# Performance work log

Hardware: AMD Instinct MI355X
Metric: run time of the kernel (lower is better)

## Reference

```python
import jax, jax.numpy as jnp
import numpy as np

H = 64        # hidden_dim
T = 3         # message passing steps
M = 3         # set2set steps
NEF = 4       # num_edge_features
NNF = 11      # num_node_features
NT = 12       # num_targets
N_NODES = 10000
N_EDGES = 50000
B = 256       # number of graphs


def setup_inputs() -> dict:
    key = jax.random.key(0)
    ks = jax.random.split(key, 32)

    def p(k, shape):
        fan_in = shape[-1]
        return jax.random.normal(k, shape, jnp.float32) / np.sqrt(fan_in)

    inp = {}
    inp['x'] = jax.random.normal(ks[0], (N_NODES, NNF), jnp.float32)
    inp['edge_attr'] = jax.random.uniform(ks[1], (N_EDGES, NEF), jnp.float32)
    inp['edge_index'] = jax.random.randint(ks[2], (2, N_EDGES), 0, N_NODES)
    inp['batch'] = jnp.sort(jax.random.randint(ks[3], (N_NODES,), 0, B))
    inp['batch_size'] = B
    # nn1: edge MLP -> per-edge HxH weight
    inp['w1a'] = p(ks[4], (H, NEF)); inp['b1a'] = jnp.zeros((H,), jnp.float32)
    inp['w1b'] = p(ks[5], (H, H));   inp['b1b'] = jnp.zeros((H,), jnp.float32)
    inp['w1c'] = p(ks[6], (H * H, H)); inp['b1c'] = jnp.zeros((H * H,), jnp.float32)
    # GRUCell
    inp['gru_wih'] = p(ks[7], (3 * H, H)); inp['gru_whh'] = p(ks[8], (3 * H, H))
    inp['gru_bih'] = jnp.zeros((3 * H,), jnp.float32); inp['gru_bhh'] = jnp.zeros((3 * H,), jnp.float32)
    # lin: (H + NNF) -> 2H
    inp['lin_w'] = p(ks[9], (2 * H, H + NNF)); inp['lin_b'] = jnp.zeros((2 * H,), jnp.float32)
    # Set2Set 2-layer LSTM: in_channels = 2H, input = 4H, hidden = 2H
    IC = 2 * H
    inp['lstm_wih0'] = p(ks[10], (4 * IC, 2 * IC)); inp['lstm_whh0'] = p(ks[11], (4 * IC, IC))
    inp['lstm_bih0'] = jnp.zeros((4 * IC,), jnp.float32); inp['lstm_bhh0'] = jnp.zeros((4 * IC,), jnp.float32)
    inp['lstm_wih1'] = p(ks[12], (4 * IC, IC)); inp['lstm_whh1'] = p(ks[13], (4 * IC, IC))
    inp['lstm_bih1'] = jnp.zeros((4 * IC,), jnp.float32); inp['lstm_bhh1'] = jnp.zeros((4 * IC,), jnp.float32)
    # nn2: 4H -> 8H -> num_targets
    inp['w2a'] = p(ks[14], (8 * H, 4 * H)); inp['b2a'] = jnp.zeros((8 * H,), jnp.float32)
    inp['w2b'] = p(ks[15], (NT, 8 * H)); inp['b2b'] = jnp.zeros((NT,), jnp.float32)
    return inp


def _gru(x, h, wih, whh, bih, bhh):
    gi = x @ wih.T + bih
    gh = h @ whh.T + bhh
    ir, iz, inn = jnp.split(gi, 3, axis=1)
    hr, hz, hn = jnp.split(gh, 3, axis=1)
    r = jax.nn.sigmoid(ir + hr)
    z = jax.nn.sigmoid(iz + hz)
    n = jnp.tanh(inn + r * hn)
    return (1.0 - z) * n + z * h


def _lstm(x, h, c, wih, whh, bih, bhh):
    g = x @ wih.T + bih + h @ whh.T + bhh
    i, f, gg, o = jnp.split(g, 4, axis=1)
    c_new = jax.nn.sigmoid(f) * c + jax.nn.sigmoid(i) * jnp.tanh(gg)
    h_new = jax.nn.sigmoid(o) * jnp.tanh(c_new)
    return h_new, c_new


def reference(x, edge_attr, w1a, b1a, w1b, b1b, w1c, b1c,
              gru_wih, gru_whh, gru_bih, gru_bhh, lin_w, lin_b,
              lstm_wih0, lstm_whh0, lstm_bih0, lstm_bhh0,
              lstm_wih1, lstm_whh1, lstm_bih1, lstm_bhh1,
              w2a, b2a, w2b, b2b, edge_index, batch, batch_size):
    N = x.shape[0]
    E = edge_attr.shape[0]
    src, dst = edge_index[0], edge_index[1]

    # pad node features into hidden state
    h = jnp.zeros((N, H), x.dtype).at[:, :x.shape[1]].set(x)

    # nn1 edge MLP -> per-edge (H, H) weight (edge_attr constant over T, hoisted)
    e1 = jax.nn.relu(edge_attr @ w1a.T + b1a)
    e1 = jax.nn.relu(e1 @ w1b.T + b1b)
    W_edge = (e1 @ w1c.T + b1c).reshape(E, H, H)  # [E, in, out]

    # T rounds of NNConv (gather -> per-edge matvec -> scatter-add) + GRU
    for _ in range(T):
        m_e = jnp.einsum('eh,eho->eo', h[src], W_edge)
        m = jax.ops.segment_sum(m_e, dst, num_segments=N)
        h = _gru(m, h, gru_wih, gru_whh, gru_bih, gru_bhh)

    h = jnp.concatenate([h, x], axis=1) @ lin_w.T + lin_b  # [N, 2H]

    # Set2Set readout with 2-layer LSTM
    IC = 2 * H
    q_star = jnp.zeros((batch_size, 2 * IC), h.dtype)
    h0 = jnp.zeros((batch_size, IC), h.dtype); c0 = jnp.zeros_like(h0)
    h1 = jnp.zeros_like(h0); c1 = jnp.zeros_like(h0)
    for _ in range(M):
        h0, c0 = _lstm(q_star, h0, c0, lstm_wih0, lstm_whh0, lstm_bih0, lstm_bhh0)
        h1, c1 = _lstm(h0, h1, c1, lstm_wih1, lstm_whh1, lstm_bih1, lstm_bhh1)
        q = h1  # [B, IC]
        e = jnp.sum(h * q[batch], axis=-1)  # [N]
        emax = jax.ops.segment_max(e, batch, num_segments=batch_size)
        a = jnp.exp(e - emax[batch])
        denom = jax.ops.segment_sum(a, batch, num_segments=batch_size)
        a = a / denom[batch]
        r = jax.ops.segment_sum(a[:, None] * h, batch, num_segments=batch_size)
        q_star = jnp.concatenate([q, r], axis=-1)  # [B, 4H]

    out = jax.nn.relu(q_star @ w2a.T + b2a) @ w2b.T + b2b
    return out
```

## Files before the change

kernel.cpp:

```cpp
#include <hip/hip_runtime.h>
#include <math.h>

#define NN 10000
#define NE 50000
#define BG 256
#define NNF 11
#define NT 12

typedef unsigned int u32;
typedef __attribute__((ext_vector_type(8))) short short8v;
typedef __attribute__((ext_vector_type(4))) float f32x4;

__device__ __forceinline__ float sigm(float x){ return 1.0f/(1.0f+__expf(-x)); }
__device__ __forceinline__ u32 f2bf(float f){
  u32 u = __float_as_uint(f);
  return (u + 0x7fffu + ((u>>16)&1u)) >> 16;
}
__device__ __forceinline__ float bf2f(u32 s){ return __uint_as_float(s<<16); }

__global__ __launch_bounds__(256) void k_h_init(const float* __restrict__ x, float* __restrict__ h,
                         unsigned short* __restrict__ hHi, unsigned short* __restrict__ hLo,
                         const float* __restrict__ b1c, float* __restrict__ hb,
                         float* __restrict__ m){
  __shared__ float sv[8][64];
  int t = threadIdx.x, w = t>>6, lane = t&63;
  int n0 = blockIdx.x*8 + w*2;
  #pragma unroll
  for (int q = 0; q < 2; ++q){
    int n = n0 + q;
    float v = (lane < NNF) ? x[n*NNF + lane] : 0.0f;
    h[n*64+lane] = v;
    u32 hv = f2bf(v);
    hHi[n*64+lane] = (unsigned short)hv;
    hLo[n*64+lane] = (unsigned short)f2bf(v - bf2f(hv));
    sv[2*w+q][lane] = v;
  }
  __syncthreads();
  #pragma unroll
  for (int q = 0; q < 2; ++q){
    int n = n0 + q;
    float acc = 0.f;
    #pragma unroll 8
    for (int i = 0; i < 64; ++i) acc = fmaf(sv[2*w+q][i], b1c[i*64+lane], acc);
    hb[n*64+lane] = acc;
    m[n*64+lane] = 0.f;
  }
}

__global__ void k_prep(const float* __restrict__ gwih, const float* __restrict__ gwhh,
                       const float* __restrict__ linw, const float* __restrict__ w1b,
                       const float* __restrict__ wih0, const float* __restrict__ whh0,
                       const float* __restrict__ wih1, const float* __restrict__ whh1,
                       const float* __restrict__ w2a,  const float* __restrict__ w1c,
                       float* __restrict__ wihT, float* __restrict__ whhT,
                       float* __restrict__ linT, unsigned short* __restrict__ w1bB,
                       float* __restrict__ p0i, float* __restrict__ p0h,
                       float* __restrict__ p1i, float* __restrict__ p1h,
                       float* __restrict__ w2aT, unsigned short* __restrict__ qtT,
                       int* __restrict__ deg, float* __restrict__ state0){
  int tid = blockIdx.x*256 + threadIdx.x;
  if (tid < 12288){ int i=tid>>6, j=tid&63; wihT[j*192+i]=gwih[tid]; return; }
  tid -= 12288;
  if (tid < 12288){ int i=tid>>6, j=tid&63; whhT[j*192+i]=gwhh[tid]; return; }
  tid -= 12288;
  if (tid < 9600){ int i=tid/75, j=tid-i*75; linT[j*128+i]=linw[tid]; return; }
  tid -= 9600;
  if (tid < 4096){ w1bB[tid] = (unsigned short)f2bf(w1b[tid]); return; }
  tid -= 4096;
  if (tid < 32768){ int i=tid>>7, j=tid&127;
    float4 v = make_float4(wih0[(j)*256+i], wih0[(128+j)*256+i],
                           wih0[(256+j)*256+i], wih0[(384+j)*256+i]);
    *(float4*)&p0i[tid*4] = v; return; }
  tid -= 32768;
  if (tid < 16384){ int i=tid>>7, j=tid&127;
    float4 v = make_float4(whh0[(j)*128+i], whh0[(128+j)*128+i],
                           whh0[(256+j)*128+i], whh0[(384+j)*128+i]);
    *(float4*)&p0h[tid*4] = v; return; }
  tid -= 16384;
  if (tid < 16384){ int i=tid>>7, j=tid&127;
    float4 v = make_float4(wih1[(j)*128+i], wih1[(128+j)*128+i],
                           wih1[(256+j)*128+i], wih1[(384+j)*128+i]);
    *(float4*)&p1i[tid*4] = v; return; }
  tid -= 16384;
  if (tid < 16384){ int i=tid>>7, j=tid&127;
    float4 v = make_float4(whh1[(j)*128+i], whh1[(128+j)*128+i],
                           whh1[(256+j)*128+i], whh1[(384+j)*128+i]);
    *(float4*)&p1h[tid*4] = v; return; }
  tid -= 16384;
  if (tid < 131072){ int i=tid>>8, j=tid&255; w2aT[j*512+i]=w2a[tid]; return; }
  tid -= 131072;
  if (tid < 262144){ int ko=tid>>6, hh=tid&63; int k=ko>>6, o=ko&63;
                     qtT[tid] = (unsigned short)f2bf(w1c[(hh*64+o)*64+k]); return; }
  tid -= 262144;
  if (tid < NN){ deg[tid] = 0; return; }
  tid -= NN;
  if (tid < 196608) state0[tid] = 0.f;
}

__global__ __launch_bounds__(256) void k_e1m(const float* __restrict__ ea,
                     const float* __restrict__ w1a, const float* __restrict__ b1a,
                     const unsigned short* __restrict__ w1bB, const float* __restrict__ b1b,
                     unsigned short* __restrict__ e1b){
  __shared__ unsigned short sHi[4][16][64], sLo[4][16][64];
  int t = threadIdx.x, w = t>>6, l = t&63;
  int c = l & 15, g = l >> 4;
  int eb = blockIdx.x*64 + w*16;
  float wa0=w1a[l*4+0], wa1=w1a[l*4+1], wa2=w1a[l*4+2], wa3=w1a[l*4+3];
  float bb1 = b1a[l];
  char* hbase = (char*)&sHi[w][0][0];
  char* lbase = (char*)&sLo[w][0][0];
  #pragma unroll
  for (int r = 0; r < 16; ++r){
    int e = eb + r; if (e >= NE) e = NE-1;
    float4 a = *(const float4*)&ea[e*4];
    float h1 = fmaxf(bb1 + a.x*wa0 + a.y*wa1 + a.z*wa2 + a.w*wa3, 0.f);
    u32 hv = f2bf(h1);
    u32 lv = f2bf(h1 - bf2f(hv));
    int wb = (r*128 + l*2) ^ ((r & 7) << 4);
    *(unsigned short*)(hbase + wb) = (unsigned short)hv;
    *(unsigned short*)(lbase + wb) = (unsigned short)lv;
  }
  __syncthreads();
  int xv = (c & 7) << 4;
  int rb0 = (c*128 + g*16) ^ xv;
  int rb1 = (c*128 + 64 + g*16) ^ xv;
  short8v aH0 = *(const short8v*)(hbase + rb0);
  short8v aH1 = *(const short8v*)(hbase + rb1);
  short8v aL0 = *(const short8v*)(lbase + rb0);
  short8v aL1 = *(const short8v*)(lbase + rb1);
  f32x4 acc[4];
  #pragma unroll
  for (int f = 0; f < 4; ++f){
    const short* wrow = (const short*)w1bB + (f*16 + c)*64 + g*8;
    short8v b0 = *(const short8v*)wrow;
    short8v b1 = *(const short8v*)(wrow + 32);
    acc[f] = f32x4{0.f,0.f,0.f,0.f};
    acc[f] = __builtin_amdgcn_mfma_f32_16x16x32_bf16(aH0, b0, acc[f], 0, 0, 0);
    acc[f] = __builtin_amdgcn_mfma_f32_16x16x32_bf16(aL0, b0, acc[f], 0, 0, 0);
    acc[f] = __builtin_amdgcn_mfma_f32_16x16x32_bf16(aH1, b1, acc[f], 0, 0, 0);
    acc[f] = __builtin_amdgcn_mfma_f32_16x16x32_bf16(aL1, b1, acc[f], 0, 0, 0);
  }
  #pragma unroll
  for (int f = 0; f < 4; ++f){
    float bb2 = b1b[f*16 + c];
    #pragma unroll
    for (int r = 0; r < 4; ++r){
      int e = eb + 4*g + r;
      if (e < NE)
        e1b[e*64 + f*16 + c] = (unsigned short)f2bf(fmaxf(acc[f][r] + bb2, 0.f));
    }
  }
}

__global__ __launch_bounds__(512) void k_P3(const unsigned short* __restrict__ hHi,
                      const unsigned short* __restrict__ hLo,
                      const unsigned short* __restrict__ qtT, u32* __restrict__ P2){
  __shared__ unsigned short sB[16384];
  int t = threadIdx.x; int w = t >> 6; int l = t & 63;
  int c = l & 15, g = l >> 4;
  int nt = blockIdx.x >> 4, kt = blockIdx.x & 15;
  int kob = kt*256;
  const char* qsrc = (const char*)qtT + (size_t)kob*128;
  char* sb = (char*)sB;
  #pragma unroll
  for (int r = 0; r < 4; ++r){
    int dstb = (r*512 + t)*16;
    int srcb = dstb ^ (((dstb >> 7) & 7) << 4);
    *(uint4*)(sb + dstb) = *(const uint4*)(qsrc + srcb);
  }
  int nb = nt*128 + w*16;
  int rowA = nb + c; if (rowA >= NN) rowA = NN-1;
  const short8v* aHiP = (const short8v*)((const short*)hHi + rowA*64 + g*8);
  const short8v* aLoP = (const short8v*)((const short*)hLo + rowA*64 + g*8);
  short8v aH0 = aHiP[0], aH1 = aHiP[4];
  short8v aL0 = aLoP[0], aL1 = aLoP[4];
  __syncthreads();
  int xv = (c & 7) << 4;
  f32x4 acc[16];
  #pragma unroll
  for (int f = 0; f < 16; ++f) acc[f] = f32x4{0.f,0.f,0.f,0.f};
  #pragma unroll
  for (int f = 0; f < 16; ++f){
    int baseb = f*2048 + c*128 + g*16;
    short8v b0 = *(const short8v*)(sb + (baseb ^ xv));
    short8v b1 = *(const short8v*)(sb + ((baseb + 64) ^ xv));
    acc[f] = __builtin_amdgcn_mfma_f32_16x16x32_bf16(aH0, b0, acc[f], 0, 0, 0);
    acc[f] = __builtin_amdgcn_mfma_f32_16x16x32_bf16(aL0, b0, acc[f], 0, 0, 0);
    acc[f] = __builtin_amdgcn_mfma_f32_16x16x32_bf16(aH1, b1, acc[f], 0, 0, 0);
    acc[f] = __builtin_amdgcn_mfma_f32_16x16x32_bf16(aL1, b1, acc[f], 0, 0, 0);
  }
  int k2b = kt*2;
  #pragma unroll
  for (int r = 0; r < 4; ++r){
    int node = nb + 4*g + r;
    if (node < NN){
      u32* dst = P2 + (size_t)node*2048;
      #pragma unroll
      for (int kk = 0; kk < 2; ++kk){
        uint4 v;
        v.x = f2bf(acc[8*kk+0][r]) | (f2bf(acc[8*kk+4][r]) << 16);
        v.y = f2bf(acc[8*kk+1][r]) | (f2bf(acc[8*kk+5][r]) << 16);
        v.z = f2bf(acc[8*kk+2][r]) | (f2bf(acc[8*kk+6][r]) << 16);
        v.w = f2bf(acc[8*kk+3][r]) | (f2bf(acc[8*kk+7][r]) << 16);
        *(uint4*)(dst + (k2b+kk)*64 + c*4) = v;
      }
    }
  }
}

__global__ void k_deg(const int* __restrict__ ei, int* __restrict__ deg){
  int e = blockIdx.x*256 + threadIdx.x;
  if (e >= NE) return;
  atomicAdd(&deg[ei[e]], 1);
}

__global__ __launch_bounds__(256) void k_scan(const int* __restrict__ deg, int* __restrict__ rowptr,
                       int* __restrict__ cursor){
  __shared__ int part[256];
  int t = threadIdx.x;
  int base = t*40;
  int s = 0;
  for (int i = 0; i < 40; ++i){ int idx = base+i; if (idx < NN) s += deg[idx]; }
  part[t] = s;
  __syncthreads();
  for (int off = 1; off < 256; off <<= 1){
    int v = (t >= off) ? part[t-off] : 0;
    __syncthreads();
    part[t] += v;
    __syncthreads();
  }
  int run = (t == 0) ? 0 : part[t-1];
  for (int i = 0; i < 40; ++i){
    int idx = base+i;
    if (idx < NN){ rowptr[idx] = run; cursor[idx] = run; run += deg[idx]; }
  }
  if (t == 255) rowptr[NN] = part[255];
}

__global__ void k_fill(const int* __restrict__ ei, int* __restrict__ cursor, int* __restrict__ csr_e){
  int e = blockIdx.x*256 + threadIdx.x;
  if (e >= NE) return;
  int s = ei[e];
  int pos = atomicAdd(&cursor[s], 1);
  csr_e[pos] = e;
}

__global__ __launch_bounds__(256, 2) void k_msg3(const int* __restrict__ rowptr,
                       const int* __restrict__ csr_e,
                       const int* __restrict__ ei, const u32* __restrict__ e1u,
                       const u32* __restrict__ P2, const float* __restrict__ hb,
                       float* __restrict__ m){
  int t = threadIdx.x; int w = t >> 6; int l = t & 63;
  int oo = ((l & 3) << 4) | (l >> 2);
  int n = blockIdx.x*4 + w;
  int jb = rowptr[n], je = rowptr[n+1];
  if (jb == je) return;
  float hbv = hb[n*64 + oo];
  const u32* Pn = P2 + (size_t)n*2048;
  u32 pr[32];
  #pragma unroll
  for (int k2 = 0; k2 < 32; ++k2) pr[k2] = Pn[k2*64 + l];
  int e = csr_e[jb];
  uint4 q[8];
  {
    const uint4* er4 = (const uint4*)(e1u + (size_t)e*32);
    #pragma unroll
    for (int i = 0; i < 8; ++i) q[i] = er4[i];
  }
  for (int j = jb; j < je; ++j){
    int dst = ei[NE + e];
    int en = (j+1 < je) ? csr_e[j+1] : e;
    uint4 qn[8];
    const uint4* ern = (const uint4*)(e1u + (size_t)en*32);
    #pragma unroll
    for (int i = 0; i < 8; ++i) qn[i] = ern[i];
    float a0 = hbv, a1 = 0.f, a2 = 0.f, a3 = 0.f;
    #pragma unroll
    for (int i = 0; i < 8; ++i){
      u32 w0 = q[i].x, w1 = q[i].y, w2 = q[i].z, w3 = q[i].w;
      u32 p0 = pr[4*i], p1 = pr[4*i+1], p2 = pr[4*i+2], p3 = pr[4*i+3];
      a0 = fmaf(bf2f(w0 & 0xffffu), bf2f(p0 & 0xffffu), a0);
      a0 = fmaf(bf2f(w0 >> 16),     bf2f(p0 >> 16),     a0);
      a1 = fmaf(bf2f(w1 & 0xffffu), bf2f(p1 & 0xffffu), a1);
      a1 = fmaf(bf2f(w1 >> 16),     bf2f(p1 >> 16),     a1);
      a2 = fmaf(bf2f(w2 & 0xffffu), bf2f(p2 & 0xffffu), a2);
      a2 = fmaf(bf2f(w2 >> 16),     bf2f(p2 >> 16),     a2);
      a3 = fmaf(bf2f(w3 & 0xffffu), bf2f(p3 & 0xffffu), a3);
      a3 = fmaf(bf2f(w3 >> 16),     bf2f(p3 >> 16),     a3);
    }
    atomicAdd(&m[dst*64 + oo], (a0+a1)+(a2+a3));
    #pragma unroll
    for (int i = 0; i < 8; ++i) q[i] = qn[i];
    e = en;
  }
}

__global__ __launch_bounds__(256) void k_gru(const float* __restrict__ m, float* __restrict__ h,
                     unsigned short* __restrict__ hHi, unsigned short* __restrict__ hLo,
                     const float* __restrict__ wihT, const float* __restrict__ whhT,
                     const float* __restrict__ bih, const float* __restrict__ bhh,
                     const float* __restrict__ b1c, float* __restrict__ hb,
                     float* __restrict__ mz){
  __shared__ float sm[8][64], sh[8][64], sv[8][64];
  int t = threadIdx.x, w = t>>6, lane = t&63;
  int n0 = blockIdx.x*8 + w*2;
  sm[2*w][lane]   = m[n0*64+lane];
  sm[2*w+1][lane] = m[(n0+1)*64+lane];
  sh[2*w][lane]   = h[n0*64+lane];
  sh[2*w+1][lane] = h[(n0+1)*64+lane];
  __syncthreads();
  float gi[2][3] = {{0,0,0},{0,0,0}}, gh[2][3] = {{0,0,0},{0,0,0}};
  #pragma unroll 2
  for (int i=0;i<64;++i){
    const float* wr = wihT + i*192;
    const float* ur = whhT + i*192;
    float w0=wr[lane], w1=wr[64+lane], w2=wr[128+lane];
    float u0=ur[lane], u1=ur[64+lane], u2=ur[128+lane];
    #pragma unroll
    for (int q=0;q<2;++q){
      float mi = sm[2*w+q][i], hi = sh[2*w+q][i];
      gi[q][0]=fmaf(mi,w0,gi[q][0]); gi[q][1]=fmaf(mi,w1,gi[q][1]); gi[q][2]=fmaf(mi,w2,gi[q][2]);
      gh[q][0]=fmaf(hi,u0,gh[q][0]); gh[q][1]=fmaf(hi,u1,gh[q][1]); gh[q][2]=fmaf(hi,u2,gh[q][2]);
    }
  }
  #pragma unroll
  for (int q=0;q<2;++q){
    int n = n0 + q;
    float r  = sigm(gi[q][0]+bih[lane]      + gh[q][0]+bhh[lane]);
    float z  = sigm(gi[q][1]+bih[64+lane]   + gh[q][1]+bhh[64+lane]);
    float nn_= tanhf(gi[q][2]+bih[128+lane] + r*(gh[q][2]+bhh[128+lane]));
    float ho = sh[2*w+q][lane];
    float hv = (1.f-z)*nn_ + z*ho;
    h[n*64+lane] = hv;
    u32 hv16 = f2bf(hv);
    hHi[n*64+lane] = (unsigned short)hv16;
    hLo[n*64+lane] = (unsigned short)f2bf(hv - bf2f(hv16));
    sv[2*w+q][lane] = hv;
  }
  __syncthreads();
  #pragma unroll
  for (int q=0;q<2;++q){
    int n = n0 + q;
    float acc = 0.f;
    #pragma unroll 8
    for (int i = 0; i < 64; ++i) acc = fmaf(sv[2*w+q][i], b1c[i*64+lane], acc);
    hb[n*64+lane] = acc;
    mz[n*64+lane] = 0.f;
  }
}

__global__ __launch_bounds__(256) void k_lin(const float* __restrict__ h, const float* __restrict__ x,
                     const float* __restrict__ linT, const float* __restrict__ lin_b, float* __restrict__ h2){
  __shared__ float sh[4][64];
  int t=threadIdx.x, w=t>>6, lane=t&63;
  int n = blockIdx.x*4 + w;
  sh[w][lane] = h[n*64+lane];
  __syncthreads();
  float a0 = lin_b[lane], a1 = lin_b[64+lane];
  #pragma unroll 4
  for (int i=0;i<64;++i){
    float v = sh[w][i];
    a0 = fmaf(v, linT[i*128+lane], a0);
    a1 = fmaf(v, linT[i*128+64+lane], a1);
  }
  #pragma unroll
  for (int i=0;i<11;++i){
    float v = x[n*NNF+i];
    a0 = fmaf(v, linT[(64+i)*128+lane], a0);
    a1 = fmaf(v, linT[(64+i)*128+64+lane], a1);
  }
  h2[n*128+lane] = a0;
  h2[n*128+64+lane] = a1;
}

__global__ void k_bounds(const int* __restrict__ batch, int* __restrict__ gstart){
  int b = blockIdx.x*256 + threadIdx.x;
  if (b > BG) return;
  int lo=0, hi=NN;
  while (lo < hi){ int mid=(lo+hi)>>1; if (batch[mid] < b) lo=mid+1; else hi=mid; }
  gstart[b]=lo;
}

__global__ __launch_bounds__(512) void k_lstm4(
    float* __restrict__ qstar,
    float* __restrict__ h0, float* __restrict__ c0,
    float* __restrict__ h1, float* __restrict__ c1,
    const f32x4* __restrict__ p0i, const f32x4* __restrict__ p0h,
    const f32x4* __restrict__ p1i, const f32x4* __restrict__ p1h,
    const float* __restrict__ bih0, const float* __restrict__ bhh0,
    const float* __restrict__ bih1, const float* __restrict__ bhh1){
  __shared__ float sq[4][256], s0[4][128], s1[4][128], sn[4][128];
  int t = threadIdx.x, g = t>>7, j = t&127;
  int b = blockIdx.x*4 + g;
  sq[t>>8][t&255]            = qstar[blockIdx.x*1024 + t];
  sq[(t+512)>>8][(t+512)&255]= qstar[blockIdx.x*1024 + 512 + t];
  s0[g][j] = h0[b*128+j];
  s1[g][j] = h1[b*128+j];
  __syncthreads();
  f32x4 A0 = f32x4{bih0[j]+bhh0[j], bih0[128+j]+bhh0[128+j],
                   bih0[256+j]+bhh0[256+j], bih0[384+j]+bhh0[384+j]};
  f32x4 A1 = f32x4{0,0,0,0}, A2 = f32x4{0,0,0,0}, A3 = f32x4{0,0,0,0};
  const float* q = sq[g];
  #pragma unroll 8
  for (int i = 0; i < 256; i += 4){
    A0 += q[i]   * p0i[(i)*128+j];
    A1 += q[i+1] * p0i[(i+1)*128+j];
    A2 += q[i+2] * p0i[(i+2)*128+j];
    A3 += q[i+3] * p0i[(i+3)*128+j];
  }
  const float* hp = s0[g];
  #pragma unroll 8
  for (int i = 0; i < 128; i += 4){
    A0 += hp[i]   * p0h[(i)*128+j];
    A1 += hp[i+1] * p0h[(i+1)*128+j];
    A2 += hp[i+2] * p0h[(i+2)*128+j];
    A3 += hp[i+3] * p0h[(i+3)*128+j];
  }
  f32x4 A = (A0+A1)+(A2+A3);
  {
    float cc = c0[b*128+j];
    float ig = sigm(A[0]), fg = sigm(A[1]), gg = tanhf(A[2]), og = sigm(A[3]);
    float cn = fg*cc + ig*gg;
    c0[b*128+j] = cn;
    float hn = og*tanhf(cn);
    h0[b*128+j] = hn;
    sn[g][j] = hn;
  }
  __syncthreads();
  f32x4 B0 = f32x4{bih1[j]+bhh1[j], bih1[128+j]+bhh1[128+j],
                   bih1[256+j]+bhh1[256+j], bih1[384+j]+bhh1[384+j]};
  f32x4 B1 = f32x4{0,0,0,0}, B2 = f32x4{0,0,0,0}, B3 = f32x4{0,0,0,0};
  const float* np = sn[g];
  const float* op = s1[g];
  #pragma unroll 8
  for (int i = 0; i < 128; i += 4){
    B0 += np[i]   * p1i[(i)*128+j];
    B1 += np[i+1] * p1i[(i+1)*128+j];
    B2 += np[i+2] * p1i[(i+2)*128+j];
    B3 += np[i+3] * p1i[(i+3)*128+j];
    B0 += op[i]   * p1h[(i)*128+j];
    B1 += op[i+1] * p1h[(i+1)*128+j];
    B2 += op[i+2] * p1h[(i+2)*128+j];
    B3 += op[i+3] * p1h[(i+3)*128+j];
  }
  f32x4 B = (B0+B1)+(B2+B3);
  {
    float cc = c1[b*128+j];
    float ig = sigm(B[0]), fg = sigm(B[1]), gg = tanhf(B[2]), og = sigm(B[3]);
    float cn = fg*cc + ig*gg;
    c1[b*128+j] = cn;
    float hn = og*tanhf(cn);
    h1[b*128+j] = hn;
    qstar[b*256+j] = hn;
  }
}

__global__ __launch_bounds__(256) void k_attn2(const float* __restrict__ h2,
                       const float* __restrict__ h1,
                       const int* __restrict__ gstart, float* __restrict__ qstar){
  __shared__ float pm[4], pl[4], pr[4][128];
  int b = blockIdx.x, t = threadIdx.x, w = t>>6, lane = t&63;
  float q0 = h1[b*128+lane], q1 = h1[b*128+64+lane];
  int s = gstart[b], e = gstart[b+1];
  float mrun = -3.0e38f, l = 0.f, r0 = 0.f, r1 = 0.f;
  for (int n = s + w; n < e; n += 4){
    float v0 = h2[n*128+lane], v1 = h2[n*128+64+lane];
    float d = fmaf(v0, q0, v1*q1);
    #pragma unroll
    for (int off = 32; off; off >>= 1) d += __shfl_xor(d, off);
    float mn = fmaxf(mrun, d);
    float sc = __expf(mrun - mn);
    float ww = __expf(d - mn);
    l = l*sc + ww;
    r0 = r0*sc + ww*v0;
    r1 = r1*sc + ww*v1;
    mrun = mn;
  }
  pr[w][lane] = r0; pr[w][64+lane] = r1;
  if (lane == 0){ pm[w] = mrun; pl[w] = l; }
  __syncthreads();
  if (t < 128){
    float M = fmaxf(fmaxf(pm[0],pm[1]), fmaxf(pm[2],pm[3]));
    float L = 0.f, R = 0.f;
    #pragma unroll
    for (int ww = 0; ww < 4; ++ww){
      float sc = __expf(pm[ww] - M);
      L = fmaf(pl[ww], sc, L);
      R = fmaf(pr[ww][t], sc, R);
    }
    float inv = (L > 0.f) ? 1.f/L : 0.f;
    qstar[b*256 + 128 + t] = R*inv;
  }
}

__global__ __launch_bounds__(512) void k_head(const float* __restrict__ qstar,
                      const float* __restrict__ w2aT, const float* __restrict__ b2a,
                      const float* __restrict__ w2b,  const float* __restrict__ b2b,
                      float* __restrict__ out){
  __shared__ float qs[256], sg[512];
  int b = blockIdx.x, j = threadIdx.x, w = j>>6, lane = j&63;
  if (j < 256) qs[j] = qstar[b*256 + j];
  __syncthreads();
  float a0 = b2a[j], a1 = 0.f, a2 = 0.f, a3 = 0.f;
  #pragma unroll
  for (int i = 0; i < 256; i += 4){
    a0 = fmaf(qs[i],   w2aT[(i)*512+j],   a0);
    a1 = fmaf(qs[i+1], w2aT[(i+1)*512+j], a1);
    a2 = fmaf(qs[i+2], w2aT[(i+2)*512+j], a2);
    a3 = fmaf(qs[i+3], w2aT[(i+3)*512+j], a3);
  }
  sg[j] = fmaxf((a0+a1)+(a2+a3), 0.f);
  __syncthreads();
  for (int jj = w; jj < NT; jj += 8){
    const float* wr = w2b + jj*512;
    float acc = 0.f;
    #pragma unroll
    for (int i = 0; i < 8; ++i) acc = fmaf(sg[lane+i*64], wr[lane+i*64], acc);
    #pragma unroll
    for (int off = 32; off; off >>= 1) acc += __shfl_xor(acc, off);
    if (lane == 0) out[b*NT+jj] = acc + b2b[jj];
  }
}

extern "C" void kernel_launch(void* const* d_in, const int* in_sizes, int n_in,
                              void* d_out, int out_size, void* d_ws, size_t ws_size,
                              hipStream_t stream) {
  const float* x    = (const float*)d_in[0];
  const float* ea   = (const float*)d_in[1];
  const int*   eidx = (const int*)d_in[2];
  const int*   batch= (const int*)d_in[3];
  const float* w1a  = (const float*)d_in[5];
  const float* b1a  = (const float*)d_in[6];
  const float* w1b  = (const float*)d_in[7];
  const float* b1b  = (const float*)d_in[8];
  const float* w1c  = (const float*)d_in[9];
  const float* b1c  = (const float*)d_in[10];
  const float* gwih = (const float*)d_in[11];
  const float* gwhh = (const float*)d_in[12];
  const float* gbih = (const float*)d_in[13];
  const float* gbhh = (const float*)d_in[14];
  const float* linw = (const float*)d_in[15];
  const float* linb = (const float*)d_in[16];
  const float* wih0 = (const float*)d_in[17];
  const float* whh0 = (const float*)d_in[18];
  const float* bih0 = (const float*)d_in[19];
  const float* bhh0 = (const float*)d_in[20];
  const float* wih1 = (const float*)d_in[21];
  const float* whh1 = (const float*)d_in[22];
  const float* bih1 = (const float*)d_in[23];
  const float* bhh1 = (const float*)d_in[24];
  const float* w2a  = (const float*)d_in[25];
  const float* b2a  = (const float*)d_in[26];
  const float* w2b  = (const float*)d_in[27];
  const float* b2b  = (const float*)d_in[28];
  float* out = (float*)d_out;

  char* p = (char*)d_ws;
  auto alloc = [&](size_t nbytes){ void* r = (void*)p; p += (nbytes + 255) & ~size_t(255); return r; };
  float* h    = (float*)alloc((size_t)NN*64*4);
  float* hb   = (float*)alloc((size_t)NN*64*4);
  float* m    = (float*)alloc((size_t)NN*64*4);
  float* h2   = (float*)alloc((size_t)NN*128*4);
  float* wihT = (float*)alloc(64*192*4);
  float* whhT = (float*)alloc(64*192*4);
  float* linT = (float*)alloc(75*128*4);
  unsigned short* w1bB = (unsigned short*)alloc(64*64*2);
  float* p0i  = (float*)alloc(131072*4);
  float* p0h  = (float*)alloc(65536*4);
  float* p1i  = (float*)alloc(65536*4);
  float* p1h  = (float*)alloc(65536*4);
  float* w2aT = (float*)alloc(256*512*4);
  float* qstar= (float*)alloc(256*256*4);
  float* h0   = (float*)alloc(256*128*4);
  float* c0   = (float*)alloc(256*128*4);
  float* h1s  = (float*)alloc(256*128*4);
  float* c1   = (float*)alloc(256*128*4);
  int*  gstart= (int*)alloc(257*4);
  unsigned short* e1b = (unsigned short*)alloc((size_t)NE*64*2);
  unsigned short* qtT = (unsigned short*)alloc((size_t)4096*64*2);
  unsigned short* hHi = (unsigned short*)alloc((size_t)NN*64*2);
  unsigned short* hLo = (unsigned short*)alloc((size_t)NN*64*2);
  int*  deg   = (int*)alloc((size_t)NN*4);
  int*  rowptr= (int*)alloc((size_t)(NN+1)*4);
  int*  cursor= (int*)alloc((size_t)NN*4);
  int*  csr_e = (int*)alloc((size_t)NE*4);
  u32*  P2    = (u32*)alloc((size_t)NN*2048*4);

  k_prep<<<2813, 256, 0, stream>>>(gwih, gwhh, linw, w1b, wih0, whh0, wih1, whh1,
                                   w2a, w1c, wihT, whhT, linT, w1bB, p0i, p0h,
                                   p1i, p1h, w2aT, qtT, deg, qstar);
  k_h_init<<<1250, 256, 0, stream>>>(x, h, hHi, hLo, b1c, hb, m);
  k_e1m<<<782, 256, 0, stream>>>(ea, w1a, b1a, w1bB, b1b, e1b);
  k_bounds<<<2, 256, 0, stream>>>(batch, gstart);
  k_deg<<<196, 256, 0, stream>>>(eidx, deg);
  k_scan<<<1, 256, 0, stream>>>(deg, rowptr, cursor);
  k_fill<<<196, 256, 0, stream>>>(eidx, cursor, csr_e);

  for (int t = 0; t < 3; ++t) {
    k_P3<<<79*16, 512, 0, stream>>>(hHi, hLo, qtT, P2);
    k_msg3<<<2500, 256, 0, stream>>>(rowptr, csr_e, eidx, (const u32*)e1b, P2, hb, m);
    k_gru<<<1250, 256, 0, stream>>>(m, h, hHi, hLo, wihT, whhT, gbih, gbhh, b1c, hb, m);
  }

  k_lin<<<2500, 256, 0, stream>>>(h, x, linT, linb, h2);

  for (int s = 0; s < 3; ++s) {
    k_lstm4<<<64, 512, 0, stream>>>(qstar, h0, c0, h1s, c1,
                                    (const f32x4*)p0i, (const f32x4*)p0h,
                                    (const f32x4*)p1i, (const f32x4*)p1h,
                                    bih0, bhh0, bih1, bhh1);
    k_attn2<<<256, 256, 0, stream>>>(h2, h1s, gstart, qstar);
  }

  k_head<<<256, 512, 0, stream>>>(qstar, w2aT, b2a, w2b, b2b, out);
}
```

Measured before the change: 598.3 us.

## Split Set2Set LSTM into two wide kernels with split-K reduction

Replaces the single 64-block LSTM kernel with two kernels (layer 0 and layer 1), each launched on 512 blocks. Each block handles two graphs and a 32-unit slice of the outputs, with the K dimension split across 8 warps and reduced through shared memory. Because blocks no longer own whole rows, h0 and h1 are ping-ponged between two buffers to avoid read/write races, and the state zeroing is extended to cover the new buffers. The aim is to use far more compute units for the latency-bound LSTM step, at the cost of an extra launch per step and more redundant weight reads.

```diff
diff --git a/kernel.cpp b/kernel.cpp
--- a/kernel.cpp
+++ b/kernel.cpp
@@ -94,7 +94,7 @@
   tid -= 262144;
   if (tid < NN){ deg[tid] = 0; return; }
   tid -= NN;
-  if (tid < 196608) state0[tid] = 0.f;
+  if (tid < 262144) state0[tid] = 0.f;
 }
 
 __global__ __launch_bounds__(256) void k_e1m(const float* __restrict__ ea,
@@ -381,77 +381,116 @@
   gstart[b]=lo;
 }
 
-__global__ __launch_bounds__(512) void k_lstm4(
-    float* __restrict__ qstar,
-    float* __restrict__ h0, float* __restrict__ c0,
-    float* __restrict__ h1, float* __restrict__ c1,
+__global__ __launch_bounds__(256) void k_lstmA(
+    const float* __restrict__ qstar, const float* __restrict__ h0r,
+    float* __restrict__ c0, float* __restrict__ h0w,
     const f32x4* __restrict__ p0i, const f32x4* __restrict__ p0h,
+    const float* __restrict__ bih0, const float* __restrict__ bhh0){
+  __shared__ float sq[512], sh[256];
+  __shared__ float red[8][2][32][5];
+  int t = threadIdx.x;
+  int gp = blockIdx.x >> 2, uq = blockIdx.x & 3;
+  int g0 = gp*2;
+  int u = t & 31, c = t >> 5;
+  int j = uq*32 + u;
+  sq[t]       = qstar[(size_t)g0*256 + t];
+  sq[t + 256] = qstar[(size_t)g0*256 + 256 + t];
+  sh[t]       = h0r[g0*128 + t];
+  __syncthreads();
+  float ai=0,af=0,ag=0,ao=0, bi=0,bf_=0,bg=0,bo=0;
+  #pragma unroll 8
+  for (int k = 0; k < 32; ++k){
+    int i = c*32 + k;
+    f32x4 w = p0i[i*128 + j];
+    float x0 = sq[i], x1 = sq[256+i];
+    ai=fmaf(x0,w[0],ai); af=fmaf(x0,w[1],af); ag=fmaf(x0,w[2],ag); ao=fmaf(x0,w[3],ao);
+    bi=fmaf(x1,w[0],bi); bf_=fmaf(x1,w[1],bf_); bg=fmaf(x1,w[2],bg); bo=fmaf(x1,w[3],bo);
+  }
+  #pragma unroll 8
+  for (int k = 0; k < 16; ++k){
+    int i = c*16 + k;
+    f32x4 w = p0h[i*128 + j];
+    float x0 = sh[i], x1 = sh[128+i];
+    ai=fmaf(x0,w[0],ai); af=fmaf(x0,w[1],af); ag=fmaf(x0,w[2],ag); ao=fmaf(x0,w[3],ao);
+    bi=fmaf(x1,w[0],bi); bf_=fmaf(x1,w[1],bf_); bg=fmaf(x1,w[2],bg); bo=fmaf(x1,w[3],bo);
+  }
+  red[c][0][u][0]=ai; red[c][0][u][1]=af; red[c][0][u][2]=ag; red[c][0][u][3]=ao;
+  red[c][1][u][0]=bi; red[c][1][u][1]=bf_; red[c][1][u][2]=bg; red[c][1][u][3]=bo;
+  __syncthreads();
+  if (t < 64){
+    int g = t >> 5, uu = t & 31;
+    int jj = uq*32 + uu;
+    float G[4];
+    #pragma unroll
+    for (int q = 0; q < 4; ++q){
+      float s = bih0[q*128 + jj] + bhh0[q*128 + jj];
+      #pragma unroll
+      for (int cc = 0; cc < 8; ++cc) s += red[cc][g][uu][q];
+      G[q] = s;
+    }
+    int idx = (g0 + g)*128 + jj;
+    float cc0 = c0[idx];
+    float ig = sigm(G[0]), fg = sigm(G[1]), gg = tanhf(G[2]), og = sigm(G[3]);
+    float cn = fg*cc0 + ig*gg;
+    c0[idx] = cn;
+    h0w[idx] = og*tanhf(cn);
+  }
+}
+
+__global__ __launch_bounds__(256) void k_lstmB(
+    const float* __restrict__ h0n, const float* __restrict__ h1r,
+    float* __restrict__ c1, float* __restrict__ h1w, float* __restrict__ qstar,
     const f32x4* __restrict__ p1i, const f32x4* __restrict__ p1h,
-    const float* __restrict__ bih0, const float* __restrict__ bhh0,
     const float* __restrict__ bih1, const float* __restrict__ bhh1){
-  __shared__ float sq[4][256], s0[4][128], s1[4][128], sn[4][128];
-  int t = threadIdx.x, g = t>>7, j = t&127;
-  int b = blockIdx.x*4 + g;
-  sq[t>>8][t&255]            = qstar[blockIdx.x*1024 + t];
-  sq[(t+512)>>8][(t+512)&255]= qstar[blockIdx.x*1024 + 512 + t];
-  s0[g][j] = h0[b*128+j];
-  s1[g][j] = h1[b*128+j];
-  __syncthreads();
-  f32x4 A0 = f32x4{bih0[j]+bhh0[j], bih0[128+j]+bhh0[128+j],
-                   bih0[256+j]+bhh0[256+j], bih0[384+j]+bhh0[384+j]};
-  f32x4 A1 = f32x4{0,0,0,0}, A2 = f32x4{0,0,0,0}, A3 = f32x4{0,0,0,0};
-  const float* q = sq[g];
+  __shared__ float s0[256], s1[256];
+  __shared__ float red[8][2][32][5];
+  int t = threadIdx.x;
+  int gp = blockIdx.x >> 2, uq = blockIdx.x & 3;
+  int g0 = gp*2;
+  int u = t & 31, c = t >> 5;
+  int j = uq*32 + u;
+  s0[t] = h0n[g0*128 + t];
+  s1[t] = h1r[g0*128 + t];
+  __syncthreads();
+  float ai=0,af=0,ag=0,ao=0, bi=0,bf_=0,bg=0,bo=0;
   #pragma unroll 8
-  for (int i = 0; i < 256; i += 4){
-    A0 += q[i]   * p0i[(i)*128+j];
-    A1 += q[i+1] * p0i[(i+1)*128+j];
-    A2 += q[i+2] * p0i[(i+2)*128+j];
-    A3 += q[i+3] * p0i[(i+3)*128+j];
-  }
-  const float* hp = s0[g];
+  for (int k = 0; k < 16; ++k){
+    int i = c*16 + k;
+    f32x4 w = p1i[i*128 + j];
+    float x0 = s0[i], x1 = s0[128+i];
+    ai=fmaf(x0,w[0],ai); af=fmaf(x0,w[1],af); ag=fmaf(x0,w[2],ag); ao=fmaf(x0,w[3],ao);
+    bi=fmaf(x1,w[0],bi); bf_=fmaf(x1,w[1],bf_); bg=fmaf(x1,w[2],bg); bo=fmaf(x1,w[3],bo);
+  }
   #pragma unroll 8
-  for (int i = 0; i < 128; i += 4){
-    A0 += hp[i]   * p0h[(i)*128+j];
-    A1 += hp[i+1] * p0h[(i+1)*128+j];
-    A2 += hp[i+2] * p0h[(i+2)*128+j];
-    A3 += hp[i+3] * p0h[(i+3)*128+j];
-  }
-  f32x4 A = (A0+A1)+(A2+A3);
-  {
-    float cc = c0[b*128+j];
-    float ig = sigm(A[0]), fg = sigm(A[1]), gg = tanhf(A[2]), og = sigm(A[3]);
-    float cn = fg*cc + ig*gg;
-    c0[b*128+j] = cn;
+  for (int k = 0; k < 16; ++k){
+    int i = c*16 + k;
+    f32x4 w = p1h[i*128 + j];
+    float x0 = s1[i], x1 = s1[128+i];
+    ai=fmaf(x0,w[0],ai); af=fmaf(x0,w[1],af); ag=fmaf(x0,w[2],ag); ao=fmaf(x0,w[3],ao);
+    bi=fmaf(x1,w[0],bi); bf_=fmaf(x1,w[1],bf_); bg=fmaf(x1,w[2],bg); bo=fmaf(x1,w[3],bo);
+  }
+  red[c][0][u][0]=ai; red[c][0][u][1]=af; red[c][0][u][2]=ag; red[c][0][u][3]=ao;
+  red[c][1][u][0]=bi; red[c][1][u][1]=bf_; red[c][1][u][2]=bg; red[c][1][u][3]=bo;
+  __syncthreads();
+  if (t < 64){
+    int g = t >> 5, uu = t & 31;
+    int jj = uq*32 + uu;
+    float G[4];
+    #pragma unroll
+    for (int q = 0; q < 4; ++q){
+      float s = bih1[q*128 + jj] + bhh1[q*128 + jj];
+      #pragma unroll
+      for (int cc = 0; cc < 8; ++cc) s += red[cc][g][uu][q];
+      G[q] = s;
+    }
+    int idx = (g0 + g)*128 + jj;
+    float cc1 = c1[idx];
+    float ig = sigm(G[0]), fg = sigm(G[1]), gg = tanhf(G[2]), og = sigm(G[3]);
+    float cn = fg*cc1 + ig*gg;
+    c1[idx] = cn;
     float hn = og*tanhf(cn);
-    h0[b*128+j] = hn;
-    sn[g][j] = hn;
-  }
-  __syncthreads();
-  f32x4 B0 = f32x4{bih1[j]+bhh1[j], bih1[128+j]+bhh1[128+j],
-                   bih1[256+j]+bhh1[256+j], bih1[384+j]+bhh1[384+j]};
-  f32x4 B1 = f32x4{0,0,0,0}, B2 = f32x4{0,0,0,0}, B3 = f32x4{0,0,0,0};
-  const float* np = sn[g];
-  const float* op = s1[g];
-  #pragma unroll 8
-  for (int i = 0; i < 128; i += 4){
-    B0 += np[i]   * p1i[(i)*128+j];
-    B1 += np[i+1] * p1i[(i+1)*128+j];
-    B2 += np[i+2] * p1i[(i+2)*128+j];
-    B3 += np[i+3] * p1i[(i+3)*128+j];
-    B0 += op[i]   * p1h[(i)*128+j];
-    B1 += op[i+1] * p1h[(i+1)*128+j];
-    B2 += op[i+2] * p1h[(i+2)*128+j];
-    B3 += op[i+3] * p1h[(i+3)*128+j];
-  }
-  f32x4 B = (B0+B1)+(B2+B3);
-  {
-    float cc = c1[b*128+j];
-    float ig = sigm(B[0]), fg = sigm(B[1]), gg = tanhf(B[2]), og = sigm(B[3]);
-    float cn = fg*cc + ig*gg;
-    c1[b*128+j] = cn;
-    float hn = og*tanhf(cn);
-    h1[b*128+j] = hn;
-    qstar[b*256+j] = hn;
+    h1w[idx] = hn;
+    qstar[(size_t)(g0 + g)*256 + jj] = hn;
   }
 }
 
@@ -575,6 +614,8 @@
   float* c0   = (float*)alloc(256*128*4);
   float* h1s  = (float*)alloc(256*128*4);
   float* c1   = (float*)alloc(256*128*4);
+  float* h0b2 = (float*)alloc(256*128*4);
+  float* h1b2 = (float*)alloc(256*128*4);
   int*  gstart= (int*)alloc(257*4);
   unsigned short* e1b = (unsigned short*)alloc((size_t)NE*64*2);
   unsigned short* qtT = (unsigned short*)alloc((size_t)4096*64*2);
@@ -586,7 +627,7 @@
   int*  csr_e = (int*)alloc((size_t)NE*4);
   u32*  P2    = (u32*)alloc((size_t)NN*2048*4);
 
-  k_prep<<<2813, 256, 0, stream>>>(gwih, gwhh, linw, w1b, wih0, whh0, wih1, whh1,
+  k_prep<<<3069, 256, 0, stream>>>(gwih, gwhh, linw, w1b, wih0, whh0, wih1, whh1,
                                    w2a, w1c, wihT, whhT, linT, w1bB, p0i, p0h,
                                    p1i, p1h, w2aT, qtT, deg, qstar);
   k_h_init<<<1250, 256, 0, stream>>>(x, h, hHi, hLo, b1c, hb, m);
@@ -605,11 +646,15 @@
   k_lin<<<2500, 256, 0, stream>>>(h, x, linT, linb, h2);
 
   for (int s = 0; s < 3; ++s) {
-    k_lstm4<<<64, 512, 0, stream>>>(qstar, h0, c0, h1s, c1,
-                                    (const f32x4*)p0i, (const f32x4*)p0h,
-                                    (const f32x4*)p1i, (const f32x4*)p1h,
-                                    bih0, bhh0, bih1, bhh1);
-    k_attn2<<<256, 256, 0, stream>>>(h2, h1s, gstart, qstar);
+    float* h0r = (s & 1) ? h0b2 : h0;
+    float* h0w = (s & 1) ? h0   : h0b2;
+    float* h1r = (s & 1) ? h1b2 : h1s;
+    float* h1w = (s & 1) ? h1s  : h1b2;
+    k_lstmA<<<512, 256, 0, stream>>>(qstar, h0r, c0, h0w, (const f32x4*)p0i,
+                                     (const f32x4*)p0h, bih0, bhh0);
+    k_lstmB<<<512, 256, 0, stream>>>(h0w, h1r, c1, h1w, qstar, (const f32x4*)p1i,
+                                     (const f32x4*)p1h, bih1, bhh1);
+    k_attn2<<<256, 256, 0, stream>>>(h2, h1w, gstart, qstar);
   }
 
   k_head<<<256, 512, 0, stream>>>(qstar, w2aT, b2a, w2b, b2b, out);
```

New measurement: 500.4 us. 16.4% less time.
